# Optimization experiments

Hardware: AMD Instinct MI355X
Metric: run time of the kernel (lower is better)

## Reference

```python
import jax, jax.numpy as jnp
import numpy as np
from jax import lax

EPS = 1e-5

def binarize_ste(x):
    # sign binarization to {-1,+1} (0 -> +1) with straight-through gradient
    s = jnp.where(x >= 0, 1.0, -1.0).astype(x.dtype)
    return x + lax.stop_gradient(s - x)

def bn(x, gamma, beta, mean, var):
    # inference-mode batchnorm; broadcast over channel axis 1 for 4D, axis 1 for 2D
    if x.ndim == 4:
        shape = (1, -1, 1, 1)
    else:
        shape = (1, -1)
    inv = gamma.reshape(shape) / jnp.sqrt(var.reshape(shape) + EPS)
    return (x - mean.reshape(shape)) * inv + beta.reshape(shape)

def conv_rep(x, w):
    # replicate (edge) padding of 1, then valid 3x3 conv, NCHW/OIHW
    xp = jnp.pad(x, ((0, 0), (0, 0), (1, 1), (1, 1)), mode='edge')
    return lax.conv_general_dilated(xp, binarize_ste(w), (1, 1), 'VALID',
                                    dimension_numbers=('NCHW', 'OIHW', 'NCHW'))

def maxpool2(x):
    return lax.reduce_window(x, -jnp.inf, lax.max, (1, 1, 2, 2), (1, 1, 2, 2), 'VALID')

def hardtanh(x):
    return jnp.clip(x, -1.0, 1.0)

def setup_inputs() -> dict:
    key = jax.random.key(0)
    ks = jax.random.split(key, 16)
    B = 2048
    inp = {
        'x': jax.random.normal(ks[0], (B, 1, 28, 28), jnp.float32),
        'conv1_w': jax.random.normal(ks[1], (64, 1, 3, 3), jnp.float32),
        'bn1_gamma': jax.random.uniform(ks[2], (64,), jnp.float32),
        'bn1_beta': jax.random.normal(ks[3], (64,), jnp.float32),
        'bn1_mean': jax.random.normal(ks[4], (64,), jnp.float32),
        'bn1_var': jax.random.uniform(ks[5], (64,), jnp.float32),
        'conv2_w': jax.random.normal(ks[6], (64, 64, 3, 3), jnp.float32),
        'bn2_gamma': jax.random.uniform(ks[7], (64,), jnp.float32),
        'bn2_beta': jax.random.normal(ks[8], (64,), jnp.float32),
        'bn2_mean': jax.random.normal(ks[9], (64,), jnp.float32),
        'bn2_var': jax.random.uniform(ks[10], (64,), jnp.float32),
        'fc1_w': jax.random.normal(ks[11], (2048, 3136), jnp.float32),
        'bn3_gamma': jax.random.uniform(ks[12], (2048,), jnp.float32),
        'bn3_beta': jax.random.normal(ks[13], (2048,), jnp.float32),
        'bn3_mean': jax.random.normal(ks[14], (2048,), jnp.float32),
        'bn3_var': jax.random.uniform(ks[15], (2048,), jnp.float32),
        'fc2_w': jax.random.normal(jax.random.fold_in(key, 99), (10, 2048), jnp.float32),
        'scale': jnp.array([0.001], jnp.float32),
    }
    return inp

def reference(x, conv1_w, bn1_gamma, bn1_beta, bn1_mean, bn1_var,
              conv2_w, bn2_gamma, bn2_beta, bn2_mean, bn2_var,
              fc1_w, bn3_gamma, bn3_beta, bn3_mean, bn3_var,
              fc2_w, scale):
    # block 1: binarized conv -> BN -> hardtanh -> binarize -> maxpool
    h = conv_rep(x, conv1_w)                          # [B,64,28,28]
    h = binarize_ste(hardtanh(bn(h, bn1_gamma, bn1_beta, bn1_mean, bn1_var)))
    h = maxpool2(h)                                   # [B,64,14,14]
    # block 2
    h = conv_rep(h, conv2_w)                          # [B,64,14,14]
    h = binarize_ste(hardtanh(bn(h, bn2_gamma, bn2_beta, bn2_mean, bn2_var)))
    h = maxpool2(h)                                   # [B,64,7,7]
    h = h.reshape(h.shape[0], -1)                     # [B,3136] (C*H*W order)
    # fc block
    h = h @ binarize_ste(fc1_w).T                     # [B,2048]
    h = binarize_ste(hardtanh(bn(h, bn3_gamma, bn3_beta, bn3_mean, bn3_var)))
    h = h @ binarize_ste(fc2_w).T                     # [B,10]
    return h * scale
```

## Files before the change

kernel.cpp:

```cpp
#include <hip/hip_runtime.h>
#include <cstdint>

#define EPS 1e-5f

typedef unsigned long long u64;
typedef unsigned int u32;
typedef unsigned short u16;
typedef unsigned char u8;
typedef float v2f __attribute__((ext_vector_type(2)));

__device__ __forceinline__ int clampi(int v, int lo, int hi) {
    return v < lo ? lo : (v > hi ? hi : v);
}

__device__ __forceinline__ v2f v2_fma(v2f a, v2f b, v2f c) {
#if __has_builtin(__builtin_elementwise_fma)
    return __builtin_elementwise_fma(a, b, c);
#else
    v2f r; r.x = __builtin_fmaf(a.x, b.x, c.x); r.y = __builtin_fmaf(a.y, b.y, c.y); return r;
#endif
}
__device__ __forceinline__ v2f v2_max(v2f a, v2f b) {
#if __has_builtin(__builtin_elementwise_max)
    return __builtin_elementwise_max(a, b);
#else
    v2f r; r.x = fmaxf(a.x, b.x); r.y = fmaxf(a.y, b.y); return r;
#endif
}


__global__ __launch_bounds__(256) void k_conv1r(
    const float* __restrict__ x,
    const float* __restrict__ conv1_w, const float* __restrict__ conv2_w,
    const float* __restrict__ fc2_w,
    const float* __restrict__ g1, const float* __restrict__ b1,
    const float* __restrict__ m1, const float* __restrict__ v1,
    const float* __restrict__ g2, const float* __restrict__ b2,
    const float* __restrict__ m2, const float* __restrict__ v2,
    v2f* __restrict__ s1d, u64* __restrict__ w2p, u64* __restrict__ w2pk,
    float4* __restrict__ bnc1, float4* __restrict__ bnc2,
    u64* __restrict__ out1,
    const float* __restrict__ fc1_w, u64* __restrict__ wp)
{
    __shared__ float ls[3136];
    int tid = threadIdx.x;
    int bid = blockIdx.x;

    if (bid < 2048) {
        int o = bid;
        const float4* row4 = (const float4*)(fc1_w + o * 3136);
        for (int i = tid; i < 784; i += 256)
            ((float4*)ls)[i] = row4[i];
        __syncthreads();
        int lane = tid & 63, wv = tid >> 6;
        for (int p = wv; p < 49; p += 4) {
            float v = ls[lane * 49 + p];
            u64 ball = __ballot(v >= 0.f);
            if (lane == 0) wp[p * 2048 + o] = ball;
        }
        return;
    }

    if (bid < 2055) {
        int t = (bid - 2048) * 256 + tid;
        if (t < 576) {
            float s = (conv1_w[t] >= 0.f) ? 1.f : -1.f;
            v2f d; d.x = s; d.y = s;
            s1d[t] = d;
        } else if (t < 1152) {
            int u = t - 576;
            int co = u / 9, tap = u % 9;
            u64 word = 0;
            for (int ci = 0; ci < 64; ci++)
                word |= (u64)(conv2_w[(co * 64 + ci) * 9 + tap] >= 0.f) << ci;
            w2p[u] = word;
        } else if (t < 1472) {
            int u = t - 1152;
            int o = u / 32, k = u % 32;
            u64 word = 0;
            for (int j = 0; j < 64; j++)
                word |= (u64)(fc2_w[o * 2048 + k * 64 + j] >= 0.f) << j;
            w2pk[u] = word;
        } else if (t < 1536) {
            int ch = t - 1472;
            bnc1[ch] = make_float4(m1[ch], g1[ch] / sqrtf(v1[ch] + EPS), b1[ch], 0.f);
        } else if (t < 1600) {
            int ch = t - 1536;
            bnc2[ch] = make_float4(m2[ch], g2[ch] / sqrtf(v2[ch] + EPS), b2[ch], 0.f);
        }
        return;
    }

    int idx2 = bid - 2055;
    int g = idx2 & 3;
    int base = g * 16;

    v2f*    lw = (v2f*)ls;
    float4* lb = (float4*)(ls + 288);
    if (tid < 144) {
        float f = conv1_w[g * 144 + tid];
        float s = (f >= 0.f) ? 1.f : -1.f;
        v2f d; d.x = s; d.y = s;
        lw[tid] = d;
    } else if (tid < 160) {
        int ch = base + (tid - 144);
        lb[tid - 144] = make_float4(m1[ch], g1[ch] / sqrtf(v1[ch] + EPS), b1[ch], 0.f);
    }
    __syncthreads();

    int idx = (idx2 >> 2) * 256 + tid;
    int b = idx / 98, q = idx % 98;
    int qi = q / 14, pj = q % 14;

    const float* xb = x + b * 784;
    int rr[6], cc[4];
    #pragma unroll
    for (int r = 0; r < 6; r++) rr[r] = clampi(4 * qi - 1 + r, 0, 27) * 28;
    #pragma unroll
    for (int c = 0; c < 4; c++) cc[c] = clampi(2 * pj - 1 + c, 0, 27);

    v2f pp[6][3];
    #pragma unroll
    for (int r = 0; r < 6; r++) {
        float p0 = xb[rr[r] + cc[0]];
        float p1 = xb[rr[r] + cc[1]];
        float p2 = xb[rr[r] + cc[2]];
        float p3 = xb[rr[r] + cc[3]];
        v2f t0; t0.x = p0; t0.y = p1; pp[r][0] = t0;
        v2f t1; t1.x = p1; t1.y = p2; pp[r][1] = t1;
        v2f t2; t2.x = p2; t2.y = p3; pp[r][2] = t2;
    }

    u32 word0 = 0, word1 = 0;
    #pragma unroll
    for (int ch = 0; ch < 16; ch++) {
        const v2f* w = lw + ch * 9;
        v2f a01 = 0.f, a23 = 0.f;
        v2f b01 = 0.f, b23 = 0.f;
        #pragma unroll
        for (int ki = 0; ki < 3; ki++)
            #pragma unroll
            for (int kj = 0; kj < 3; kj++) {
                v2f ww = w[ki * 3 + kj];
                a01 = v2_fma(pp[ki][kj],     ww, a01);
                a23 = v2_fma(pp[ki + 1][kj], ww, a23);
                b01 = v2_fma(pp[ki + 2][kj], ww, b01);
                b23 = v2_fma(pp[ki + 3][kj], ww, b23);
            }
        float4 c4 = lb[ch];
        v2f mxA = v2_max(a01, a23);
        float vmaxA = fmaxf(mxA.x, mxA.y);
        int bitA = (((vmaxA - c4.x) * c4.y + c4.z) >= 0.f);
        word0 |= (u32)bitA << ch;
        v2f mxB = v2_max(b01, b23);
        float vmaxB = fmaxf(mxB.x, mxB.y);
        int bitB = (((vmaxB - c4.x) * c4.y + c4.z) >= 0.f);
        word1 |= (u32)bitB << ch;
    }
    int p0 = (2 * qi) * 14 + pj;
    ((u16*)out1)[(b * 196 + p0) * 4 + g]      = (u16)word0;
    ((u16*)out1)[(b * 196 + p0 + 14) * 4 + g] = (u16)word1;
}


__global__ __launch_bounds__(256) void k_conv2(
    const u64* __restrict__ in, const u64* __restrict__ w2p,
    const float4* __restrict__ bnc2, u64* __restrict__ out2)
{
    int tid = threadIdx.x;
    int g = blockIdx.y;
    int base = g * 8;

    int idx = blockIdx.x * 256 + tid;
    int b = idx / 49, p = idx % 49;
    int pi = p / 7, pj = p % 7;

    const u64* ib = in + b * 196;
    int rr[4], cc[4];
    #pragma unroll
    for (int r = 0; r < 4; r++) rr[r] = clampi(2 * pi - 1 + r, 0, 13) * 14;
    #pragma unroll
    for (int c = 0; c < 4; c++) cc[c] = clampi(2 * pj - 1 + c, 0, 13);
    u64 a[4][4];
    #pragma unroll
    for (int r = 0; r < 4; r++)
        #pragma unroll
        for (int c = 0; c < 4; c++)
            a[r][c] = ib[rr[r] + cc[c]];

    u32 word = 0;
    #pragma unroll
    for (int co = 0; co < 8; co++) {
        const u64* w = w2p + (base + co) * 9;
        int s00 = 0, s01 = 0, s10 = 0, s11 = 0;
        #pragma unroll
        for (int ki = 0; ki < 3; ki++)
            #pragma unroll
            for (int kj = 0; kj < 3; kj++) {
                u64 ww = w[ki * 3 + kj];
                s00 += __popcll(a[ki][kj] ^ ww);
                s01 += __popcll(a[ki][kj + 1] ^ ww);
                s10 += __popcll(a[ki + 1][kj] ^ ww);
                s11 += __popcll(a[ki + 1][kj + 1] ^ ww);
            }
        int smin = min(min(s00, s01), min(s10, s11));
        float4 c4 = bnc2[base + co];
        int bit = (((float)(576 - 2 * smin) - c4.x) * c4.y + c4.z >= 0.f);
        word |= (u32)bit << co;
    }
    ((u8*)out2)[idx * 8 + g] = (u8)word;
}


#define NB 16

__global__ __launch_bounds__(256) void k_fc1(
    const u64* __restrict__ act, const u64* __restrict__ wp,
    const float* __restrict__ g, const float* __restrict__ bt,
    const float* __restrict__ mn, const float* __restrict__ vr,
    u64* __restrict__ out3)
{
    int tid = threadIdx.x;
    int btile = blockIdx.x >> 3;
    int otile = blockIdx.x & 7;
    int b0 = btile * NB;
    int o = otile * 256 + tid;
    const u64* ab = act + b0 * 49;

    int sums[NB];
    #pragma unroll
    for (int i = 0; i < NB; i++) sums[i] = 0;

    for (int p = 0; p < 49; p++) {
        u64 w = wp[p * 2048 + o];
        #pragma unroll
        for (int bb = 0; bb < NB; bb++)
            sums[bb] += __popcll(ab[bb * 49 + p] ^ w);
    }

    float iv = g[o] / sqrtf(vr[o] + EPS);
    float m = mn[o], be = bt[o];
    #pragma unroll
    for (int bb = 0; bb < NB; bb++) {
        float y = ((float)(3136 - 2 * sums[bb]) - m) * iv + be;
        u64 ball = __ballot(y >= 0.f);
        if ((tid & 63) == 0) out3[(b0 + bb) * 32 + (o >> 6)] = ball;
    }
}


__global__ void k_fc2(const u64* __restrict__ act, const u64* __restrict__ w2,
                      const float* __restrict__ scale, float* __restrict__ out)
{
    int idx = blockIdx.x * 256 + threadIdx.x;
    if (idx >= 2048 * 16) return;
    int b = idx >> 4, o = idx & 15;
    if (o >= 10) return;
    int s = 0;
    #pragma unroll
    for (int k = 0; k < 32; k++)
        s += __popcll(act[b * 32 + k] ^ w2[o * 32 + k]);
    out[b * 10 + o] = scale[0] * (float)(2048 - 2 * s);
}


extern "C" void kernel_launch(void* const* d_in, const int* in_sizes, int n_in,
                              void* d_out, int out_size, void* d_ws, size_t ws_size,
                              hipStream_t stream) {
    const float* x        = (const float*)d_in[0];
    const float* conv1_w  = (const float*)d_in[1];
    const float* bn1_g    = (const float*)d_in[2];
    const float* bn1_b    = (const float*)d_in[3];
    const float* bn1_m    = (const float*)d_in[4];
    const float* bn1_v    = (const float*)d_in[5];
    const float* conv2_w  = (const float*)d_in[6];
    const float* bn2_g    = (const float*)d_in[7];
    const float* bn2_b    = (const float*)d_in[8];
    const float* bn2_m    = (const float*)d_in[9];
    const float* bn2_v    = (const float*)d_in[10];
    const float* fc1_w    = (const float*)d_in[11];
    const float* bn3_g    = (const float*)d_in[12];
    const float* bn3_b    = (const float*)d_in[13];
    const float* bn3_m    = (const float*)d_in[14];
    const float* bn3_v    = (const float*)d_in[15];
    const float* fc2_w    = (const float*)d_in[16];
    const float* scale    = (const float*)d_in[17];
    float* out = (float*)d_out;

    char* ws = (char*)d_ws;
    v2f*    s1d  = (v2f*)   (ws + 0);
    u64*    w2p  = (u64*)   (ws + 4608);
    float4* bnc1 = (float4*)(ws + 9216);
    float4* bnc2 = (float4*)(ws + 10240);
    u64*    w2pk = (u64*)   (ws + 11264);
    u64*    wp   = (u64*)   (ws + 16384);
    u64*    out1 = (u64*)   (ws + 819200);
    u64*    out2 = (u64*)   (ws + 4030464);
    u64*    out3 = (u64*)   (ws + 4833280);

    hipLaunchKernelGGL(k_conv1r, dim3(2048 + 7 + 3136), dim3(256), 0, stream,
                       x, conv1_w, conv2_w, fc2_w,
                       bn1_g, bn1_b, bn1_m, bn1_v,
                       bn2_g, bn2_b, bn2_m, bn2_v,
                       s1d, w2p, w2pk, bnc1, bnc2,
                       out1, fc1_w, wp);
    hipLaunchKernelGGL(k_conv2, dim3(392, 8), dim3(256), 0, stream,
                       out1, w2p, bnc2, out2);
    hipLaunchKernelGGL(k_fc1, dim3(1024), dim3(256), 0, stream,
                       out2, wp, bn3_g, bn3_b, bn3_m, bn3_v, out3);
    hipLaunchKernelGGL(k_fc2, dim3(128), dim3(256), 0, stream,
                       out3, w2pk, scale, out);
}
```

Measured before the change: 200.8 us.

## Fuse fc2 into fc1 via atomic partial sums and last-block finalize

Removes the separate fc2 kernel. Each fc1 block computes partial popcount dot products for its 256-output slice against the packed fc2 weights and atomically adds them into a per-sample accumulator. A per-batch-tile counter lets the last of the 8 contributing blocks write the scaled final outputs. The accumulator and counters are zeroed by extra blocks appended to the conv2 launch. This saves a kernel launch and the out3 round trip, at the cost of atomics, fences and extra syncs inside fc1.

Measured after the change: 258.3 us. +28.6%, slower.

```diff
diff --git a/kernel.cpp b/kernel.cpp
--- a/kernel.cpp
+++ b/kernel.cpp
@@ -165,13 +165,24 @@
 
 __global__ __launch_bounds__(256) void k_conv2(
     const u64* __restrict__ in, const u64* __restrict__ w2p,
-    const float4* __restrict__ bnc2, u64* __restrict__ out2)
+    const float4* __restrict__ bnc2, u64* __restrict__ out2,
+    u32* __restrict__ accz)
 {
     int tid = threadIdx.x;
+    int bx = blockIdx.x;
+    if (bx >= 392) {
+        if (blockIdx.y == 0) {
+            int t = (bx - 392) * 256 + tid;
+            for (int i = t; i < 20608; i += 2816)
+                accz[i] = 0u;
+        }
+        return;
+    }
+
     int g = blockIdx.y;
     int base = g * 8;
 
-    int idx = blockIdx.x * 256 + tid;
+    int idx = bx * 256 + tid;
     int b = idx / 49, p = idx % 49;
     int pi = p / 7, pj = p % 7;
 
@@ -218,8 +229,11 @@
     const u64* __restrict__ act, const u64* __restrict__ wp,
     const float* __restrict__ g, const float* __restrict__ bt,
     const float* __restrict__ mn, const float* __restrict__ vr,
-    u64* __restrict__ out3)
+    const u64* __restrict__ w2pk, const float* __restrict__ scale,
+    u32* __restrict__ acc, u32* __restrict__ cnt, float* __restrict__ out)
 {
+    __shared__ u64 sball[NB][4];
+    __shared__ int sflag;
     int tid = threadIdx.x;
     int btile = blockIdx.x >> 3;
     int otile = blockIdx.x & 7;
@@ -244,23 +258,36 @@
     for (int bb = 0; bb < NB; bb++) {
         float y = ((float)(3136 - 2 * sums[bb]) - m) * iv + be;
         u64 ball = __ballot(y >= 0.f);
-        if ((tid & 63) == 0) out3[(b0 + bb) * 32 + (o >> 6)] = ball;
-    }
-}
-
-
-__global__ void k_fc2(const u64* __restrict__ act, const u64* __restrict__ w2,
-                      const float* __restrict__ scale, float* __restrict__ out)
-{
-    int idx = blockIdx.x * 256 + threadIdx.x;
-    if (idx >= 2048 * 16) return;
-    int b = idx >> 4, o = idx & 15;
-    if (o >= 10) return;
-    int s = 0;
-    #pragma unroll
-    for (int k = 0; k < 32; k++)
-        s += __popcll(act[b * 32 + k] ^ w2[o * 32 + k]);
-    out[b * 10 + o] = scale[0] * (float)(2048 - 2 * s);
+        if ((tid & 63) == 0) sball[bb][tid >> 6] = ball;
+    }
+    __syncthreads();
+
+    if (tid < NB * 10) {
+        int bb = tid / 10, o2 = tid % 10;
+        const u64* w2 = w2pk + o2 * 32 + otile * 4;
+        int s = 0;
+        #pragma unroll
+        for (int k = 0; k < 4; k++)
+            s += __popcll(sball[bb][k] ^ w2[k]);
+        __hip_atomic_fetch_add(&acc[(b0 + bb) * 10 + o2], (u32)s,
+                               __ATOMIC_RELAXED, __HIP_MEMORY_SCOPE_AGENT);
+        __threadfence();
+    }
+    __syncthreads();
+
+    if (tid == 0) {
+        u32 old = __hip_atomic_fetch_add(&cnt[btile], 1u,
+                                         __ATOMIC_ACQ_REL, __HIP_MEMORY_SCOPE_AGENT);
+        sflag = (old == 7u);
+    }
+    __syncthreads();
+
+    if (sflag && tid < NB * 10) {
+        int bb = tid / 10, o2 = tid % 10;
+        u32 s = __hip_atomic_load(&acc[(b0 + bb) * 10 + o2],
+                                  __ATOMIC_ACQUIRE, __HIP_MEMORY_SCOPE_AGENT);
+        out[(b0 + bb) * 10 + o2] = scale[0] * (float)(2048 - 2 * (int)s);
+    }
 }
 
 
@@ -296,7 +323,8 @@
     u64*    wp   = (u64*)   (ws + 16384);
     u64*    out1 = (u64*)   (ws + 819200);
     u64*    out2 = (u64*)   (ws + 4030464);
-    u64*    out3 = (u64*)   (ws + 4833280);
+    u32*    acc  = (u32*)   (ws + 4833280);
+    u32*    cnt  = (u32*)   (ws + 4915200);
 
     hipLaunchKernelGGL(k_conv1r, dim3(2048 + 7 + 3136), dim3(256), 0, stream,
                        x, conv1_w, conv2_w, fc2_w,
@@ -304,10 +332,9 @@
                        bn2_g, bn2_b, bn2_m, bn2_v,
                        s1d, w2p, w2pk, bnc1, bnc2,
                        out1, fc1_w, wp);
-    hipLaunchKernelGGL(k_conv2, dim3(392, 8), dim3(256), 0, stream,
-                       out1, w2p, bnc2, out2);
+    hipLaunchKernelGGL(k_conv2, dim3(392 + 11, 8), dim3(256), 0, stream,
+                       out1, w2p, bnc2, out2, acc);
     hipLaunchKernelGGL(k_fc1, dim3(1024), dim3(256), 0, stream,
-                       out2, wp, bn3_g, bn3_b, bn3_m, bn3_v, out3);
-    hipLaunchKernelGGL(k_fc2, dim3(128), dim3(256), 0, stream,
-                       out3, w2pk, scale, out);
-}
+                       out2, wp, bn3_g, bn3_b, bn3_m, bn3_v,
+                       w2pk, scale, acc, cnt, out);
+}
```
